# Kernel tuning notes

Hardware: AMD Instinct MI355X
Metric: run time of the kernel (lower is better)

The kernel has to match this reference:

```python
import jax, jax.numpy as jnp
import numpy as np

B, S, H = 2, 4096, 1024
NKH, NVH, DK, DV = 8, 16, 64, 64
KEY_DIM = NKH * DK
VAL_DIM = NVH * DV
CONV_DIM = 2 * KEY_DIM + VAL_DIM
KSZ = 4
EPS = 1e-6


def setup_inputs() -> dict:
    key = jax.random.key(0)
    ks = jax.random.split(key, 8)
    s = 0.02
    return {
        "hidden_states": jax.random.normal(ks[0], (B, S, H), jnp.float32),
        "W_qkv": jax.random.normal(ks[1], (CONV_DIM, H), jnp.float32) * s,
        "conv_w": jax.random.normal(ks[2], (CONV_DIM, 1, KSZ), jnp.float32) * 0.1,
        "W_z": jax.random.normal(ks[3], (VAL_DIM, H), jnp.float32) * s,
        "W_b": jax.random.normal(ks[4], (NVH, H), jnp.float32) * s,
        "W_a": jax.random.normal(ks[5], (NVH, H), jnp.float32) * s,
        "dt_bias": jnp.ones((NVH,), jnp.float32),
        "A_log": jnp.log(jax.random.uniform(ks[6], (NVH,), jnp.float32, 0.1, 16.0)),
        "norm_weight": jnp.ones((DV,), jnp.float32),
        "W_out": jax.random.normal(ks[7], (H, VAL_DIM), jnp.float32) * s,
    }


def _forward(hidden_states, W_qkv, conv_w, W_z, W_b, W_a, dt_bias, A_log, norm_weight, W_out):
    b, s, _ = hidden_states.shape
    # fused qkv projection -> depthwise causal conv -> silu
    mixed = hidden_states @ W_qkv.T                       # [b,s,conv_dim]
    x = mixed.transpose(0, 2, 1)                          # [b,conv_dim,s]
    y = jax.lax.conv_general_dilated(
        x, conv_w, (1,), [(KSZ - 1, 0)],
        dimension_numbers=("NCH", "OIH", "NCH"),
        feature_group_count=CONV_DIM)                     # causal: left pad k-1
    mixed = jax.nn.silu(y).transpose(0, 2, 1)             # [b,s,conv_dim]

    z = (hidden_states @ W_z.T).reshape(b, s, NVH, DV)
    beta = jax.nn.sigmoid(hidden_states @ W_b.T)          # [b,s,nvh]
    a = hidden_states @ W_a.T
    g = -jnp.exp(A_log) * jax.nn.softplus(a + dt_bias)    # [b,s,nvh]

    q, k, v = jnp.split(mixed, [KEY_DIM, 2 * KEY_DIM], axis=-1)
    q = q.reshape(b, s, NKH, DK)
    k = k.reshape(b, s, NKH, DK)
    v = v.reshape(b, s, NVH, DV)
    rep = NVH // NKH
    if rep > 1:  # GQA: repeat_interleave along head dim
        q = jnp.repeat(q, rep, axis=2)
        k = jnp.repeat(k, rep, axis=2)
    q = q * (DK ** -0.5)

    # gated delta-rule recurrence over time (state: [b,h,dk,dv])
    def step(Sst, inp):
        q_t, k_t, v_t, g_t, b_t = inp                     # [b,h,dk],[b,h,dk],[b,h,dv],[b,h],[b,h]
        Sst = Sst * jnp.exp(g_t)[..., None, None]
        kv = jnp.einsum("bhkv,bhk->bhv", Sst, k_t)
        delta = (v_t - kv) * b_t[..., None]
        Sst = Sst + k_t[..., None] * delta[..., None, :]
        o = jnp.einsum("bhkv,bhk->bhv", Sst, q_t)
        return Sst, o

    S0 = jnp.zeros((b, NVH, DK, DV), jnp.float32)
    xs = (q.transpose(1, 0, 2, 3), k.transpose(1, 0, 2, 3), v.transpose(1, 0, 2, 3),
          g.transpose(1, 0, 2), beta.transpose(1, 0, 2))
    _, o = jax.lax.scan(step, S0, xs)                     # o: [s,b,h,dv]
    o = o.transpose(1, 0, 2, 3)                           # [b,s,h,dv]

    # gated RMSNorm over head_v_dim: x * silu(z), rmsnorm, * weight
    h_ = o * jax.nn.silu(z)
    var = jnp.mean(h_ * h_, axis=-1, keepdims=True)
    h_ = h_ * jax.lax.rsqrt(var + EPS) * norm_weight

    return h_.reshape(b, s, VAL_DIM) @ W_out.T            # [b,s,hidden]


def reference(hidden_states, W_qkv, conv_w, W_z, W_b, W_a, dt_bias, A_log, norm_weight, W_out):
    return _forward(hidden_states, W_qkv, conv_w, W_z, W_b, W_a, dt_bias, A_log, norm_weight, W_out)
```

## Files before the change

### kernel.cpp

```cpp
#include <hip/hip_runtime.h>
#include <hip/hip_bf16.h>
#include <stdint.h>

#define B_    2
#define S_    4096
#define H_    1024
#define NKH_  8
#define NVH_  16
#define DK_   64
#define DV_   64
#define KEYD_ 512
#define CDIM_ 2048
#define VALD_ 1024
#define NCHUNK_ 64
#define CS_   64

using bf16 = __hip_bfloat16;
using bf16x8 = __attribute__((ext_vector_type(8))) short;
using f32x4  = __attribute__((ext_vector_type(4))) float;

__device__ inline float bsh2f(short s) {
  union { ushort u; bf16 h; } c; c.u = (ushort)s; return __bfloat162float(c.h);
}
__device__ inline short f2bsh(float f) {
  union { ushort u; bf16 h; } c; c.h = __float2bfloat16(f); return (short)c.u;
}

__global__ __launch_bounds__(256) void castf2b(const float* __restrict__ x,
                                               bf16* __restrict__ y, long n) {
  const long i = ((long)blockIdx.x * 256 + threadIdx.x) * 4;
  if (i >= n) return;
  float4 v = *(const float4*)(x + i);
  union { ushort4 u; bf16 h[4]; } o;
  o.h[0] = __float2bfloat16(v.x);
  o.h[1] = __float2bfloat16(v.y);
  o.h[2] = __float2bfloat16(v.z);
  o.h[3] = __float2bfloat16(v.w);
  *(ushort4*)(y + i) = o.u;
}

template <typename OT>
__global__ __launch_bounds__(256) void gemm_bt(const bf16* __restrict__ A,
                                               const bf16* __restrict__ Bm,
                                               OT* __restrict__ C,
                                               int M, int N, int K) {
  __shared__ short Asm[128 * 32];
  __shared__ short Bsm[128 * 32];
  const int t = threadIdx.x;
  const int w = t >> 6, l = t & 63;
  const int ntn = N >> 7;
  const int bm = blockIdx.x / ntn, bn = blockIdx.x % ntn;
  const int m0 = bm << 7, n0 = bn << 7;
  const int wm = (w >> 1) << 6, wn = (w & 1) << 6;

  f32x4 acc[4][4] = {};

  const int srow = t >> 2;
  const int scol8 = (t & 3) << 3;
  const bf16* Ag = A + (long)(m0 + srow) * K + scol8;
  const bf16* Bg = Bm + (long)(n0 + srow) * K + scol8;
  const long rstep = (long)64 * K;

  const int lm = l & 15;
  const int kk = (l >> 4) << 3;
  const short* ar0 = &Asm[(wm + lm) * 32 + kk];
  const short* br0 = &Bsm[(wn + lm) * 32 + kk];

  for (int k0 = 0; k0 < K; k0 += 32) {
    bf16x8 a0 = *(const bf16x8*)(Ag + k0);
    bf16x8 a1 = *(const bf16x8*)(Ag + k0 + rstep);
    bf16x8 b0 = *(const bf16x8*)(Bg + k0);
    bf16x8 b1 = *(const bf16x8*)(Bg + k0 + rstep);
    __syncthreads();
    *(bf16x8*)&Asm[srow * 32 + scol8]        = a0;
    *(bf16x8*)&Asm[(64 + srow) * 32 + scol8] = a1;
    *(bf16x8*)&Bsm[srow * 32 + scol8]        = b0;
    *(bf16x8*)&Bsm[(64 + srow) * 32 + scol8] = b1;
    __syncthreads();
    bf16x8 af[4], bfr[4];
#pragma unroll
    for (int mi = 0; mi < 4; ++mi) af[mi] = *(const bf16x8*)(ar0 + mi * 16 * 32);
#pragma unroll
    for (int ni = 0; ni < 4; ++ni) bfr[ni] = *(const bf16x8*)(br0 + ni * 16 * 32);
#pragma unroll
    for (int mi = 0; mi < 4; ++mi)
#pragma unroll
      for (int ni = 0; ni < 4; ++ni)
        acc[mi][ni] = __builtin_amdgcn_mfma_f32_16x16x32_bf16(af[mi], bfr[ni],
                                                              acc[mi][ni], 0, 0, 0);
  }

  const int r0 = (l >> 4) << 2;
  const int cn = l & 15;
#pragma unroll
  for (int mi = 0; mi < 4; ++mi)
#pragma unroll
    for (int ni = 0; ni < 4; ++ni) {
      long base = (long)(m0 + wm + mi * 16 + r0) * N + (n0 + wn + ni * 16 + cn);
#pragma unroll
      for (int r = 0; r < 4; ++r) {
        if constexpr (sizeof(OT) == 2)
          C[base + (long)r * N] = __float2bfloat16(acc[mi][ni][r]);
        else
          C[base + (long)r * N] = acc[mi][ni][r];
      }
    }
}

__global__ __launch_bounds__(256) void conv2(const bf16* __restrict__ mixed,
                                             const float* __restrict__ cw,
                                             bf16* __restrict__ qkv) {
  const long idx = (long)blockIdx.x * 256 + threadIdx.x;
  const int c = (int)(idx & (CDIM_ - 1));
  const long row = idx >> 11;
  const int s = (int)(row & (S_ - 1));
  float acc = 0.f;
#pragma unroll
  for (int j = 0; j < 4; ++j) {
    const int ss = s - 3 + j;
    if (ss >= 0)
      acc = fmaf(cw[c * 4 + j], (float)mixed[(row + j - 3) * CDIM_ + c], acc);
  }
  float y = acc / (1.f + __expf(-acc));
  if (c < KEYD_) y *= 0.125f;
  union { uint16_t u; bf16 h; } o; o.h = __float2bfloat16(y);
  ((uint16_t*)qkv)[row * CDIM_ + c] = o.u;
}

__global__ __launch_bounds__(256) void proj_ba2(const float* __restrict__ hs,
                                                const float* __restrict__ Wb,
                                                const float* __restrict__ Wa,
                                                const float* __restrict__ dtb,
                                                const float* __restrict__ Alog,
                                                float* __restrict__ beta,
                                                float* __restrict__ g) {
  __shared__ float4 hrow[8][257];
  const long row0 = (long)blockIdx.x * 8;
  const int tid = threadIdx.x;
  for (int i = tid; i < 2048; i += 256) {
    const int r = i >> 8, c4 = i & 255;
    hrow[r][c4] = *(const float4*)(hs + (row0 + r) * H_ + (long)c4 * 4);
  }
  __syncthreads();
  const int j = tid >> 3, r = tid & 7;
  const float4* Wp = (const float4*)(j < 16 ? Wb + (long)j * H_
                                            : Wa + (long)(j - 16) * H_);
  float4 a4 = {0.f, 0.f, 0.f, 0.f};
#pragma unroll 4
  for (int i = 0; i < 256; ++i) {
    const float4 w = Wp[i];
    const float4 hv = hrow[r][i];
    a4.x = fmaf(w.x, hv.x, a4.x);
    a4.y = fmaf(w.y, hv.y, a4.y);
    a4.z = fmaf(w.z, hv.z, a4.z);
    a4.w = fmaf(w.w, hv.w, a4.w);
  }
  const float acc = (a4.x + a4.y) + (a4.z + a4.w);
  const long row = row0 + r;
  if (j < 16) {
    beta[row * NVH_ + j] = 1.f / (1.f + __expf(-acc));
  } else {
    const int hh = j - 16;
    const float x = acc + dtb[hh];
    const float sp = (x > 20.f) ? x : log1pf(__expf(x));
    g[row * NVH_ + hh] = -__expf(Alog[hh]) * sp;
  }
}

__global__ __launch_bounds__(256) void chunk_pre(const bf16* __restrict__ qkv,
                                                 const float* __restrict__ beta,
                                                 const float* __restrict__ g,
                                                 bf16* __restrict__ Wws,
                                                 bf16* __restrict__ U0ws,
                                                 float* __restrict__ lgws,
                                                 bf16* __restrict__ McT,
                                                 bf16* __restrict__ Bc) {
  __shared__ short Ksm[64][72];
  __shared__ short Vsm[64][72];
  __shared__ float Tsm[64][64];
  __shared__ short KpT[64][72];
  __shared__ float Xl[128][67];
  __shared__ float lgs[64];
  __shared__ float bts[64];
  __shared__ float belg[64];

  const int blk = blockIdx.x;
  const int hb = blk & 31, c = blk >> 5;
  const long task = (long)hb * 64 + c;
  const int h = hb & 15, b = hb >> 4, kh = h >> 1;
  const long t0 = (long)b * S_ + (long)c * CS_;
  const int tid = threadIdx.x;
  const int wv = tid >> 6, l = tid & 63;
  const int lm = l & 15, lk8 = (l >> 4) << 3;
  const int r0 = (l >> 4) << 2, cn = l & 15;
  const int srow = tid >> 2, scol = (tid & 3) * 16;

  {
    const bf16* kp = qkv + (t0 + srow) * CDIM_ + KEYD_ + kh * 64 + scol;
    const bf16* vp = qkv + (t0 + srow) * CDIM_ + 2 * KEYD_ + h * 64 + scol;
    *(bf16x8*)&Ksm[srow][scol]     = *(const bf16x8*)(kp);
    *(bf16x8*)&Ksm[srow][scol + 8] = *(const bf16x8*)(kp + 8);
    *(bf16x8*)&Vsm[srow][scol]     = *(const bf16x8*)(vp);
    *(bf16x8*)&Vsm[srow][scol + 8] = *(const bf16x8*)(vp + 8);
  }
  if (tid < 64) {
    bts[tid] = beta[(t0 + tid) * NVH_ + tid * 0 + h];
    lgs[tid] = g[(t0 + tid) * NVH_ + h];
  }
  __syncthreads();

  if (tid < 64) {
    float x = lgs[tid];
#pragma unroll
    for (int d = 1; d < 64; d <<= 1) {
      const float y = __shfl_up(x, d);
      if (tid >= d) x += y;
    }
    lgs[tid] = x;
    belg[tid] = bts[tid] * __expf(x);
  }
  __syncthreads();

  if (tid < 128) {
    f32x4 acc[2][4] = {};
#pragma unroll
    for (int ks = 0; ks < 2; ++ks) {
      bf16x8 bfr[4];
#pragma unroll
      for (int ni = 0; ni < 4; ++ni)
        bfr[ni] = *(const bf16x8*)&Ksm[ni * 16 + lm][lk8 + ks * 32];
#pragma unroll
      for (int mi = 0; mi < 2; ++mi) {
        bf16x8 afr = *(const bf16x8*)&Ksm[(wv * 2 + mi) * 16 + lm][lk8 + ks * 32];
#pragma unroll
        for (int ni = 0; ni < 4; ++ni)
          acc[mi][ni] = __builtin_amdgcn_mfma_f32_16x16x32_bf16(afr, bfr[ni],
                                                                acc[mi][ni], 0, 0, 0);
      }
    }
#pragma unroll
    for (int mi = 0; mi < 2; ++mi)
#pragma unroll
      for (int ni = 0; ni < 4; ++ni)
#pragma unroll
        for (int r = 0; r < 4; ++r) {
          const int t = (wv * 2 + mi) * 16 + r0 + r;
          const int i = ni * 16 + cn;
          Tsm[t][i] = (i < t) ? bts[t] * __expf(lgs[t] - lgs[i]) * acc[mi][ni][r]
                              : 0.f;
        }
  } else {
    const int idx = tid - 128;
    const int tt = idx >> 1;
    const int o2 = (idx & 1) * 32;
    const float dec = __expf(lgs[63] - lgs[tt]);
#pragma unroll 8
    for (int k = 0; k < 32; ++k)
      KpT[o2 + k][tt] = f2bsh(dec * bsh2f(Ksm[tt][o2 + k]));
  }
  __syncthreads();

  if (tid < 128) {
    const int colW = tid & 63;
    const bool isW = tid < 64;
#pragma unroll 8
    for (int t = 0; t < CS_; ++t)
      Xl[tid][t] = isW ? belg[t] * bsh2f(Ksm[t][colW])
                       : bts[t] * bsh2f(Vsm[t][colW]);
    for (int j = 0; j < CS_; j += 8) {
      float xs[8];
#pragma unroll
      for (int a = 0; a < 8; ++a) xs[a] = Xl[tid][j + a];
#pragma unroll
      for (int a = 1; a < 8; ++a)
#pragma unroll
        for (int bb = 0; bb < a; ++bb)
          xs[a] = fmaf(-Tsm[j + a][j + bb], xs[bb], xs[a]);
#pragma unroll
      for (int a = 1; a < 8; ++a) Xl[tid][j + a] = xs[a];
#pragma unroll 2
      for (int t = j + 8; t < CS_; ++t) {
        const float4 ta = *(const float4*)&Tsm[t][j];
        const float4 tb = *(const float4*)&Tsm[t][j + 4];
        float v = Xl[tid][t];
        v = fmaf(-ta.x, xs[0], v); v = fmaf(-ta.y, xs[1], v);
        v = fmaf(-ta.z, xs[2], v); v = fmaf(-ta.w, xs[3], v);
        v = fmaf(-tb.x, xs[4], v); v = fmaf(-tb.y, xs[5], v);
        v = fmaf(-tb.z, xs[6], v); v = fmaf(-tb.w, xs[7], v);
        Xl[tid][t] = v;
      }
    }
  }
  if (tid < 64) lgws[task * 64 + tid] = lgs[tid];
  __syncthreads();

  short (*WT)[72] = (short (*)[72]) & Tsm[0][0];
  short (*U0T)[72] = Vsm;
  if (tid < 128) {
    const int colW = tid & 63;
    const bool isW = tid < 64;
    bf16* dst = (isW ? Wws : U0ws) + task * 4096 + colW;
    short (*XT)[72] = isW ? WT : U0T;
#pragma unroll 4
    for (int t = 0; t < CS_; t += 2) {
      const float v0 = Xl[tid][t], v1 = Xl[tid][t + 1];
      dst[(long)t * 64] = __float2bfloat16(v0);
      dst[(long)(t + 1) * 64] = __float2bfloat16(v1);
      short2 pk; pk.x = f2bsh(v0); pk.y = f2bsh(v1);
      *(short2*)&XT[colW][t] = pk;
    }
  }
  __syncthreads();

  {
    f32x4 macc[4] = {};
#pragma unroll
    for (int ks = 0; ks < 2; ++ks) {
      bf16x8 afr = *(const bf16x8*)&KpT[wv * 16 + lm][lk8 + ks * 32];
#pragma unroll
      for (int ni = 0; ni < 4; ++ni) {
        bf16x8 bfr = *(const bf16x8*)&WT[ni * 16 + lm][lk8 + ks * 32];
        macc[ni] = __builtin_amdgcn_mfma_f32_16x16x32_bf16(afr, bfr, macc[ni], 0, 0, 0);
      }
    }
#pragma unroll
    for (int ni = 0; ni < 4; ++ni)
#pragma unroll
      for (int r = 0; r < 4; ++r)
        McT[task * 4096 + (wv * 16 + r0 + r) * 64 + ni * 16 + cn] =
            __float2bfloat16(-macc[ni][r]);
  }
  {
    f32x4 bacc[4] = {};
#pragma unroll
    for (int ks = 0; ks < 2; ++ks) {
      bf16x8 afr = *(const bf16x8*)&U0T[wv * 16 + lm][lk8 + ks * 32];
#pragma unroll
      for (int ni = 0; ni < 4; ++ni) {
        bf16x8 bfr = *(const bf16x8*)&KpT[ni * 16 + lm][lk8 + ks * 32];
        bacc[ni] = __builtin_amdgcn_mfma_f32_16x16x32_bf16(afr, bfr, bacc[ni], 0, 0, 0);
      }
    }
#pragma unroll
    for (int ni = 0; ni < 4; ++ni)
#pragma unroll
      for (int r = 0; r < 4; ++r)
        Bc[task * 4096 + (wv * 16 + r0 + r) * 64 + ni * 16 + cn] =
            __float2bfloat16(bacc[ni][r]);
  }
}

__global__ __launch_bounds__(256) void chunk_state(const bf16* __restrict__ McT,
                                                   const bf16* __restrict__ Bc,
                                                   const float* __restrict__ lgws,
                                                   bf16* __restrict__ Sb) {
  __shared__ short Msm[3][64][72];
  __shared__ short Bsm[3][64][72];
  __shared__ short Ssm[64][72];
  __shared__ float lgb[3];

  const int hb = blockIdx.x;
  const int tid = threadIdx.x, wv = tid >> 6, l = tid & 63;
  const int lm = l & 15, lk8 = (l >> 4) << 3;
  const int r0 = (l >> 4) << 2, cn = l & 15;
  const int srow = tid >> 2, scol = (tid & 3) * 16;

  for (int i = tid; i < 64 * 72; i += 256) ((short*)Ssm)[i] = 0;
  f32x4 Sreg[4] = {};

  auto stage = [&](int cc, int bu) {
    const long tt = (long)hb * 64 + cc;
    const bf16* mp = McT + tt * 4096 + srow * 64 + scol;
    const bf16* bp = Bc + tt * 4096 + srow * 64 + scol;
    *(bf16x8*)&Msm[bu][srow][scol]     = *(const bf16x8*)(mp);
    *(bf16x8*)&Msm[bu][srow][scol + 8] = *(const bf16x8*)(mp + 8);
    *(bf16x8*)&Bsm[bu][srow][scol]     = *(const bf16x8*)(bp);
    *(bf16x8*)&Bsm[bu][srow][scol + 8] = *(const bf16x8*)(bp + 8);
    if (tid == 0) lgb[bu] = lgws[tt * 64 + 63];
  };
  stage(0, 0);
  stage(1, 1);

  for (int c = 0; c < NCHUNK_; ++c) {
    __syncthreads();
    if (c + 2 < NCHUNK_) stage(c + 2, (c + 2) % 3);
    const int bu = c % 3;

    {
      bf16* sp = Sb + ((long)hb * 64 + c) * 4096;
#pragma unroll
      for (int ni = 0; ni < 4; ++ni)
#pragma unroll
        for (int r = 0; r < 4; ++r)
          sp[(wv * 16 + r0 + r) * 64 + ni * 16 + cn] = __float2bfloat16(Sreg[ni][r]);
    }

    bf16x8 sfr0 = *(const bf16x8*)&Ssm[wv * 16 + lm][lk8];
    bf16x8 sfr1 = *(const bf16x8*)&Ssm[wv * 16 + lm][lk8 + 32];
    f32x4 kacc[4] = {};
#pragma unroll
    for (int ni = 0; ni < 4; ++ni) {
      bf16x8 b0 = *(const bf16x8*)&Msm[bu][ni * 16 + lm][lk8];
      kacc[ni] = __builtin_amdgcn_mfma_f32_16x16x32_bf16(sfr0, b0, kacc[ni], 0, 0, 0);
      bf16x8 b1 = *(const bf16x8*)&Msm[bu][ni * 16 + lm][lk8 + 32];
      kacc[ni] = __builtin_amdgcn_mfma_f32_16x16x32_bf16(sfr1, b1, kacc[ni], 0, 0, 0);
    }
    const float eend = __expf(lgb[bu]);
#pragma unroll
    for (int ni = 0; ni < 4; ++ni)
#pragma unroll
      for (int r = 0; r < 4; ++r) {
        const float bv = bsh2f(Bsm[bu][wv * 16 + r0 + r][ni * 16 + cn]);
        Sreg[ni][r] = eend * Sreg[ni][r] + kacc[ni][r] + bv;
        Ssm[wv * 16 + r0 + r][ni * 16 + cn] = f2bsh(Sreg[ni][r]);
      }
  }
}

__global__ __launch_bounds__(256) void chunk_out(const bf16* __restrict__ qkv,
                                                 const bf16* __restrict__ Wws,
                                                 const bf16* __restrict__ U0ws,
                                                 const float* __restrict__ lgws,
                                                 const bf16* __restrict__ Sb,
                                                 float* __restrict__ o) {
  __shared__ short Qsm[64][72];
  __shared__ short Ksm[64][72];
  __shared__ short Wsm[64][72];
  __shared__ short Usm[64][72];
  __shared__ short Amm[64][72];
  __shared__ short Dsm[64][72];
  __shared__ float lgs[64];

  const int blk = blockIdx.x;
  const int hb = blk & 31, c = blk >> 5;
  const long task = (long)hb * 64 + c;
  const int h = hb & 15, b = hb >> 4, kh = h >> 1;
  const long sb = (long)b * S_ + (long)c * CS_;
  const int tid = threadIdx.x, wv = tid >> 6, l = tid & 63;
  const int lm = l & 15, lk8 = (l >> 4) << 3;
  const int r0 = (l >> 4) << 2, cn = l & 15;
  const int srow = tid >> 2, scol = (tid & 3) * 16;

  const bf16* sp = Sb + task * 4096 + (wv * 16 + lm) * 64 + lk8;
  bf16x8 sfr0 = *(const bf16x8*)(sp);
  bf16x8 sfr1 = *(const bf16x8*)(sp + 32);

  {
    const bf16* qp = qkv + (sb + srow) * CDIM_ + kh * 64 + scol;
    const bf16* kp = qkv + (sb + srow) * CDIM_ + KEYD_ + kh * 64 + scol;
    const bf16* wp = Wws + task * 4096 + srow * 64 + scol;
    const bf16* up = U0ws + task * 4096 + srow * 64 + scol;
    *(bf16x8*)&Qsm[srow][scol]     = *(const bf16x8*)(qp);
    *(bf16x8*)&Qsm[srow][scol + 8] = *(const bf16x8*)(qp + 8);
    *(bf16x8*)&Ksm[srow][scol]     = *(const bf16x8*)(kp);
    *(bf16x8*)&Ksm[srow][scol + 8] = *(const bf16x8*)(kp + 8);
    *(bf16x8*)&Wsm[srow][scol]     = *(const bf16x8*)(wp);
    *(bf16x8*)&Wsm[srow][scol + 8] = *(const bf16x8*)(wp + 8);
    *(bf16x8*)&Usm[srow][scol]     = *(const bf16x8*)(up);
    *(bf16x8*)&Usm[srow][scol + 8] = *(const bf16x8*)(up + 8);
    if (tid < 64) lgs[tid] = lgws[task * 64 + tid];
  }
  __syncthreads();

  {
    f32x4 aacc[4] = {};
#pragma unroll
    for (int ks = 0; ks < 2; ++ks) {
      bf16x8 qa = *(const bf16x8*)&Qsm[wv * 16 + lm][lk8 + ks * 32];
#pragma unroll
      for (int ni = 0; ni < 4; ++ni) {
        bf16x8 kb = *(const bf16x8*)&Ksm[ni * 16 + lm][lk8 + ks * 32];
        aacc[ni] = __builtin_amdgcn_mfma_f32_16x16x32_bf16(qa, kb, aacc[ni], 0, 0, 0);
      }
    }
#pragma unroll
    for (int ni = 0; ni < 4; ++ni)
#pragma unroll
      for (int r = 0; r < 4; ++r) {
        const int t = wv * 16 + r0 + r, i = ni * 16 + cn;
        Amm[t][i] = f2bsh((i <= t) ? aacc[ni][r] * __expf(lgs[t] - lgs[i]) : 0.f);
      }
  }
  __syncthreads();

  {
    const float sc = __expf(lgs[srow]);
#pragma unroll
    for (int j = 0; j < 16; ++j)
      Qsm[srow][scol + j] = f2bsh(sc * bsh2f(Qsm[srow][scol + j]));
  }
  __syncthreads();

  {
    f32x4 dacc[4] = {};
#pragma unroll
    for (int ni = 0; ni < 4; ++ni) {
      bf16x8 w0 = *(const bf16x8*)&Wsm[ni * 16 + lm][lk8];
      dacc[ni] = __builtin_amdgcn_mfma_f32_16x16x32_bf16(sfr0, w0, dacc[ni], 0, 0, 0);
      bf16x8 w1 = *(const bf16x8*)&Wsm[ni * 16 + lm][lk8 + 32];
      dacc[ni] = __builtin_amdgcn_mfma_f32_16x16x32_bf16(sfr1, w1, dacc[ni], 0, 0, 0);
    }
#pragma unroll
    for (int ni = 0; ni < 4; ++ni)
#pragma unroll
      for (int r = 0; r < 4; ++r) {
        const int t = ni * 16 + cn, v = r0 + r;
        Dsm[wv * 16 + v][t] = f2bsh(bsh2f(Usm[t][wv * 16 + v]) - dacc[ni][r]);
      }
  }
  bf16x8 dfr0 = *(const bf16x8*)&Dsm[wv * 16 + lm][lk8];
  bf16x8 dfr1 = *(const bf16x8*)&Dsm[wv * 16 + lm][lk8 + 32];

  {
    f32x4 oacc[4] = {};
#pragma unroll
    for (int mi = 0; mi < 4; ++mi) {
      bf16x8 q0 = *(const bf16x8*)&Qsm[mi * 16 + lm][lk8];
      oacc[mi] = __builtin_amdgcn_mfma_f32_16x16x32_bf16(q0, sfr0, oacc[mi], 0, 0, 0);
      bf16x8 q1 = *(const bf16x8*)&Qsm[mi * 16 + lm][lk8 + 32];
      oacc[mi] = __builtin_amdgcn_mfma_f32_16x16x32_bf16(q1, sfr1, oacc[mi], 0, 0, 0);
    }
#pragma unroll
    for (int mi = 0; mi < 4; ++mi) {
      bf16x8 a0 = *(const bf16x8*)&Amm[mi * 16 + lm][lk8];
      oacc[mi] = __builtin_amdgcn_mfma_f32_16x16x32_bf16(a0, dfr0, oacc[mi], 0, 0, 0);
      bf16x8 a1 = *(const bf16x8*)&Amm[mi * 16 + lm][lk8 + 32];
      oacc[mi] = __builtin_amdgcn_mfma_f32_16x16x32_bf16(a1, dfr1, oacc[mi], 0, 0, 0);
    }
#pragma unroll
    for (int mi = 0; mi < 4; ++mi)
#pragma unroll
      for (int r = 0; r < 4; ++r) {
        const int t = mi * 16 + r0 + r;
        o[(sb + t) * VALD_ + h * 64 + wv * 16 + cn] = oacc[mi][r];
      }
  }
}

__global__ __launch_bounds__(256) void gnorm2(const float* __restrict__ o,
                                              const float* __restrict__ z,
                                              const float* __restrict__ nw,
                                              bf16* __restrict__ hn) {
  const long idx = (long)blockIdx.x * 256 + threadIdx.x;
  const float* op = o + idx * 64;
  const float* zp = z + idx * 64;
  float hv[64];
  float ss = 0.f;
#pragma unroll
  for (int i = 0; i < 64; ++i) {
    const float zz = zp[i];
    const float hh = op[i] * (zz / (1.f + __expf(-zz)));
    hv[i] = hh;
    ss = fmaf(hh, hh, ss);
  }
  const float r = rsqrtf(ss * (1.f / 64.f) + 1e-6f);
#pragma unroll
  for (int i = 0; i < 64; ++i)
    hn[idx * 64 + i] = __float2bfloat16(hv[i] * r * nw[i]);
}

extern "C" void kernel_launch(void* const* d_in, const int* in_sizes, int n_in,
                              void* d_out, int out_size, void* d_ws, size_t ws_size,
                              hipStream_t stream) {
  float* out = (float*)d_out;
  const int M = B_ * S_;

  int ih, iqkv, icw, iz, ib, ia, idtb, ialog, inw, iout;
  if (n_in >= 10 && in_sizes[0] == 8388608) {
    ih = 0; iqkv = 1; icw = 2; iz = 3; ib = 4; ia = 5;
    idtb = 6; ialog = 7; inw = 8; iout = 9;
  } else {
    ih = iqkv = icw = iz = ib = ia = idtb = ialog = inw = iout = -1;
    for (int i = 0; i < n_in; ++i) {
      switch (in_sizes[i]) {
        case 8388608: ih = i; break;
        case 2097152: iqkv = i; break;
        case 8192:    icw = i; break;
        case 64:      inw = i; break;
        case 1048576: if (iz < 0) iz = i; else iout = i; break;
        case 16384:   if (ib < 0) ib = i; else ia = i; break;
        case 16:      if (idtb < 0) idtb = i; else ialog = i; break;
        default: break;
      }
    }
  }
  const float* hs   = (const float*)d_in[ih];
  const float* Wqkv = (const float*)d_in[iqkv];
  const float* cw   = (const float*)d_in[icw];
  const float* Wz   = (const float*)d_in[iz];
  const float* Wb   = (const float*)d_in[ib];
  const float* Wa   = (const float*)d_in[ia];
  const float* dtb  = (const float*)d_in[idtb];
  const float* Alog = (const float*)d_in[ialog];
  const float* nwv  = (const float*)d_in[inw];
  const float* Wout = (const float*)d_in[iout];

  char* p = (char*)d_ws;
  bf16*  mixed = (bf16*)p;
  float* of    = (float*)p;
  bf16*  McTw  = (bf16*)p;
  bf16*  Bcw   = (bf16*)(p + (size_t)2048 * 4096 * 2);
  p += (size_t)M * CDIM_ * 2;
  bf16*  hs_b  = (bf16*)p;
  bf16*  qkvb  = (bf16*)p;
  bf16*  hn    = (bf16*)p; p += (size_t)M * CDIM_ * 2;
  bf16*  Wqkv_b= (bf16*)p; p += (size_t)CDIM_ * H_ * 2;
  bf16*  Wz_b  = (bf16*)p; p += (size_t)H_ * H_ * 2;
  bf16*  Wout_b= (bf16*)p; p += (size_t)H_ * H_ * 2;
  float* betaf = (float*)p; p += (size_t)M * NVH_ * 4;
  float* gf    = (float*)p; p += (size_t)M * NVH_ * 4;
  bf16*  Wws   = (bf16*)p; p += (size_t)2048 * 4096 * 2;
  bf16*  U0ws  = (bf16*)p; p += (size_t)2048 * 4096 * 2;
  float* lgws  = (float*)p; p += (size_t)2048 * 64 * 4;
  bf16*  Sbw   = (bf16*)p; p += (size_t)2048 * 4096 * 2;
  float* zb    = out;

  {
    long n;
    n = (long)M * H_;     castf2b<<<(int)(n / 4 / 256), 256, 0, stream>>>(hs,   hs_b,   n);
    n = (long)CDIM_ * H_; castf2b<<<(int)(n / 4 / 256), 256, 0, stream>>>(Wqkv, Wqkv_b, n);
    n = (long)H_ * H_;    castf2b<<<(int)(n / 4 / 256), 256, 0, stream>>>(Wz,   Wz_b,   n);
    n = (long)H_ * H_;    castf2b<<<(int)(n / 4 / 256), 256, 0, stream>>>(Wout, Wout_b, n);
  }
  gemm_bt<bf16><<<(M / 128) * (CDIM_ / 128), 256, 0, stream>>>(hs_b, Wqkv_b, mixed, M, CDIM_, H_);
  gemm_bt<float><<<(M / 128) * (H_ / 128), 256, 0, stream>>>(hs_b, Wz_b, zb, M, H_, H_);
  proj_ba2<<<M / 8, 256, 0, stream>>>(hs, Wb, Wa, dtb, Alog, betaf, gf);
  conv2<<<(int)(((long)M * CDIM_) / 256), 256, 0, stream>>>(mixed, cw, qkvb);
  chunk_pre<<<2048, 256, 0, stream>>>(qkvb, betaf, gf, Wws, U0ws, lgws, McTw, Bcw);
  chunk_state<<<32, 256, 0, stream>>>(McTw, Bcw, lgws, Sbw);
  chunk_out<<<2048, 256, 0, stream>>>(qkvb, Wws, U0ws, lgws, Sbw, of);
  gnorm2<<<(M * NVH_) / 256, 256, 0, stream>>>(of, zb, nwv, hn);
  gemm_bt<float><<<(M / 128) * (H_ / 128), 256, 0, stream>>>(hn, Wout_b, out, M, H_, H_);
}
```

Before: 552.6 us.

## Use direct global-to-LDS loads in GEMM and blocked MFMA triangular solve

The GEMM tile load now uses global_load_lds to write 16-byte chunks straight into shared memory, skipping the register staging step. In chunk_pre, the 64x64 forward substitution is split into two 32-row halves. The off-diagonal block update between them runs as a bf16 MFMA instead of scalar FMAs. This cuts serial ALU work in the solve but adds extra syncs and a bf16 rounding step in the intermediate update, which may affect accuracy.

```diff
diff --git a/kernel.cpp b/kernel.cpp
--- a/kernel.cpp
+++ b/kernel.cpp
@@ -24,6 +24,12 @@
 }
 __device__ inline short f2bsh(float f) {
   union { ushort u; bf16 h; } c; c.h = __float2bfloat16(f); return (short)c.u;
+}
+
+__device__ __forceinline__ void gload16(const bf16* g, short* lds) {
+  __builtin_amdgcn_global_load_lds(
+      (const __attribute__((address_space(1))) void*)g,
+      (__attribute__((address_space(3))) void*)lds, 16, 0, 0);
 }
 
 __global__ __launch_bounds__(256) void castf2b(const float* __restrict__ x,
@@ -55,11 +61,10 @@
 
   f32x4 acc[4][4] = {};
 
-  const int srow = t >> 2;
-  const int scol8 = (t & 3) << 3;
-  const bf16* Ag = A + (long)(m0 + srow) * K + scol8;
-  const bf16* Bg = Bm + (long)(n0 + srow) * K + scol8;
-  const long rstep = (long)64 * K;
+  const int grow = l >> 2;
+  const int gc8 = (l & 3) << 3;
+  const bf16* Agl = A + (long)m0 * K + gc8;
+  const bf16* Bgl = Bm + (long)n0 * K + gc8;
 
   const int lm = l & 15;
   const int kk = (l >> 4) << 3;
@@ -67,15 +72,13 @@
   const short* br0 = &Bsm[(wn + lm) * 32 + kk];
 
   for (int k0 = 0; k0 < K; k0 += 32) {
-    bf16x8 a0 = *(const bf16x8*)(Ag + k0);
-    bf16x8 a1 = *(const bf16x8*)(Ag + k0 + rstep);
-    bf16x8 b0 = *(const bf16x8*)(Bg + k0);
-    bf16x8 b1 = *(const bf16x8*)(Bg + k0 + rstep);
     __syncthreads();
-    *(bf16x8*)&Asm[srow * 32 + scol8]        = a0;
-    *(bf16x8*)&Asm[(64 + srow) * 32 + scol8] = a1;
-    *(bf16x8*)&Bsm[srow * 32 + scol8]        = b0;
-    *(bf16x8*)&Bsm[(64 + srow) * 32 + scol8] = b1;
+#pragma unroll
+    for (int j = 0; j < 2; ++j) {
+      const int s = w * 2 + j;
+      gload16(Agl + (long)(s * 16 + grow) * K + k0, &Asm[s * 16 * 32]);
+      gload16(Bgl + (long)(s * 16 + grow) * K + k0, &Bsm[s * 16 * 32]);
+    }
     __syncthreads();
     bf16x8 af[4], bfr[4];
 #pragma unroll
@@ -184,6 +187,11 @@
   __shared__ float bts[64];
   __shared__ float belg[64];
 
+  short (*XB)[36]   = (short (*)[36]) & Vsm[0][0];
+  short (*TloB)[40] = (short (*)[40]) & Ksm[0][0];
+  short (*WT)[72]   = (short (*)[72]) & Tsm[0][0];
+  short (*U0T)[72]  = Vsm;
+
   const int blk = blockIdx.x;
   const int hb = blk & 31, c = blk >> 5;
   const long task = (long)hb * 64 + c;
@@ -204,7 +212,7 @@
     *(bf16x8*)&Vsm[srow][scol + 8] = *(const bf16x8*)(vp + 8);
   }
   if (tid < 64) {
-    bts[tid] = beta[(t0 + tid) * NVH_ + tid * 0 + h];
+    bts[tid] = beta[(t0 + tid) * NVH_ + h];
     lgs[tid] = g[(t0 + tid) * NVH_ + h];
   }
   __syncthreads();
@@ -260,6 +268,33 @@
   }
   __syncthreads();
 
+  auto solve32 = [&](int base) {
+    for (int j = base; j < base + 32; j += 8) {
+      float xs[8];
+#pragma unroll
+      for (int a = 0; a < 8; ++a) xs[a] = Xl[tid][j + a];
+#pragma unroll
+      for (int a = 1; a < 8; ++a)
+#pragma unroll
+        for (int bb = 0; bb < a; ++bb)
+          xs[a] = fmaf(-Tsm[j + a][j + bb], xs[bb], xs[a]);
+#pragma unroll
+      for (int a = 1; a < 8; ++a) Xl[tid][j + a] = xs[a];
+      const int tend = base + 32;
+#pragma unroll 2
+      for (int tt = j + 8; tt < tend; ++tt) {
+        const float4 ta = *(const float4*)&Tsm[tt][j];
+        const float4 tb = *(const float4*)&Tsm[tt][j + 4];
+        float v = Xl[tid][tt];
+        v = fmaf(-ta.x, xs[0], v); v = fmaf(-ta.y, xs[1], v);
+        v = fmaf(-ta.z, xs[2], v); v = fmaf(-ta.w, xs[3], v);
+        v = fmaf(-tb.x, xs[4], v); v = fmaf(-tb.y, xs[5], v);
+        v = fmaf(-tb.z, xs[6], v); v = fmaf(-tb.w, xs[7], v);
+        Xl[tid][tt] = v;
+      }
+    }
+  };
+
   if (tid < 128) {
     const int colW = tid & 63;
     const bool isW = tid < 64;
@@ -267,35 +302,46 @@
     for (int t = 0; t < CS_; ++t)
       Xl[tid][t] = isW ? belg[t] * bsh2f(Ksm[t][colW])
                        : bts[t] * bsh2f(Vsm[t][colW]);
-    for (int j = 0; j < CS_; j += 8) {
-      float xs[8];
-#pragma unroll
-      for (int a = 0; a < 8; ++a) xs[a] = Xl[tid][j + a];
-#pragma unroll
-      for (int a = 1; a < 8; ++a)
-#pragma unroll
-        for (int bb = 0; bb < a; ++bb)
-          xs[a] = fmaf(-Tsm[j + a][j + bb], xs[bb], xs[a]);
-#pragma unroll
-      for (int a = 1; a < 8; ++a) Xl[tid][j + a] = xs[a];
-#pragma unroll 2
-      for (int t = j + 8; t < CS_; ++t) {
-        const float4 ta = *(const float4*)&Tsm[t][j];
-        const float4 tb = *(const float4*)&Tsm[t][j + 4];
-        float v = Xl[tid][t];
-        v = fmaf(-ta.x, xs[0], v); v = fmaf(-ta.y, xs[1], v);
-        v = fmaf(-ta.z, xs[2], v); v = fmaf(-ta.w, xs[3], v);
-        v = fmaf(-tb.x, xs[4], v); v = fmaf(-tb.y, xs[5], v);
-        v = fmaf(-tb.z, xs[6], v); v = fmaf(-tb.w, xs[7], v);
-        Xl[tid][t] = v;
-      }
-    }
+    solve32(0);
   }
   if (tid < 64) lgws[task * 64 + tid] = lgs[tid];
   __syncthreads();
 
-  short (*WT)[72] = (short (*)[72]) & Tsm[0][0];
-  short (*U0T)[72] = Vsm;
+  {
+    const int col = tid & 127, uh = (tid >> 7) * 16;
+#pragma unroll
+    for (int u = 0; u < 16; ++u)
+      XB[col][uh + u] = f2bsh(Xl[col][uh + u]);
+  }
+  if (tid < 128) {
+    const int m = tid >> 2, u0 = (tid & 3) * 8;
+#pragma unroll
+    for (int u = 0; u < 8; ++u)
+      TloB[m][u0 + u] = f2bsh(Tsm[32 + m][u0 + u]);
+  }
+  __syncthreads();
+
+  {
+#pragma unroll
+    for (int ni2 = 0; ni2 < 2; ++ni2) {
+      const int ni = wv * 2 + ni2;
+      bf16x8 bfr = *(const bf16x8*)&XB[ni * 16 + lm][lk8];
+#pragma unroll
+      for (int mi = 0; mi < 2; ++mi) {
+        bf16x8 afr = *(const bf16x8*)&TloB[mi * 16 + lm][lk8];
+        f32x4 uacc = {};
+        uacc = __builtin_amdgcn_mfma_f32_16x16x32_bf16(afr, bfr, uacc, 0, 0, 0);
+#pragma unroll
+        for (int r = 0; r < 4; ++r)
+          Xl[ni * 16 + cn][32 + mi * 16 + r0 + r] -= uacc[r];
+      }
+    }
+  }
+  __syncthreads();
+
+  if (tid < 128) solve32(32);
+  __syncthreads();
+
   if (tid < 128) {
     const int colW = tid & 63;
     const bool isW = tid < 64;
```

After: 534.4 us. 3.3% less time.
